# Kernel tuning notes

Hardware: AMD Instinct MI355X
Metric: run time of the kernel (lower is better)

Reference implementation:

```python
import jax, jax.numpy as jnp
import numpy as np

EPS = 1e-10


def setup_inputs() -> dict:
    key = jax.random.key(0)
    ks = jax.random.split(key, 8)
    N, C, H, W = 32, 512, 14, 14
    D, HID = 2048, 256
    s1 = 1.0 / np.sqrt(C + D)
    s2 = 1.0 / np.sqrt(HID)
    return {
        "local_feature": jax.random.normal(ks[0], (N, C, H, W), jnp.float32),
        "global_feature": jax.random.normal(ks[1], (N, D, 1, 1), jnp.float32),
        "W1": jax.random.normal(ks[2], (C + D, HID), jnp.float32) * s1,
        "b1": jnp.zeros((HID,), jnp.float32),
        "W2": jax.random.normal(ks[3], (HID, HID), jnp.float32) * s2,
        "b2": jnp.zeros((HID,), jnp.float32),
        "W3": jax.random.normal(ks[4], (HID, 1), jnp.float32) * s2,
        "b3": jnp.zeros((1,), jnp.float32),
    }


def reference(local_feature, global_feature, W1, b1, W2, b2, W3, b3):
    # Vectorized form of DMIEstimator.calculate_mi (the per-sample Python loop
    # collapsed into one batched pass with a block-diagonal negative mask).
    N, C, H, W = local_feature.shape
    hw = H * W
    nhw = N * hw
    D = global_feature.shape[1]

    lf = jnp.transpose(local_feature, (0, 2, 3, 1)).reshape(nhw, C)   # [nhw, C]
    gf = global_feature[:, :, 0, 0]                                   # [N, D]

    # combined = cat([global, local], -1); split the first Linear accordingly
    # so the [N*nhw, C+D] concat tensor is never materialized.
    h_loc = lf @ W1[D:]                        # [nhw, HID]
    h_glb = gf @ W1[:D] + b1                   # [N, HID]
    h1 = jax.nn.relu(h_glb[:, None, :] + h_loc[None, :, :])  # [N, nhw, HID]
    h2 = jax.nn.relu(h1 @ W2 + b2)                            # [N, nhw, HID]
    scores = (h2 @ W3)[..., 0] + b3[0]                        # [N, nhw]

    mx = jnp.max(scores, axis=1, keepdims=True)               # [N, 1]
    ex = jnp.exp(scores - mx)

    # negatives for sample i exclude its own hw block [hw*i, hw*(i+1))
    own = (jnp.arange(nhw)[None, :] // hw) == jnp.arange(N)[:, None]  # [N, nhw]
    neg_mean = jnp.where(own, 0.0, ex).sum(axis=1) / (nhw - hw) + EPS  # [N]

    # positive (diagonal) block of scores: scores[i, hw*i : hw*(i+1)]
    pos = scores.reshape(N, N, hw)[jnp.arange(N), jnp.arange(N)]       # [N, hw]

    mi = pos - mx - jnp.log(neg_mean)[:, None]                         # [N, hw]
    return mi.reshape(N, H, W)
```

## Files before the change

kernel.cpp:

```cpp
#include <hip/hip_runtime.h>
#include <math.h>

#define NB   32
#define CC   512
#define DD   2048
#define HWP  196
#define NHW  6272
#define HID  256

typedef _Float16 h8 __attribute__((ext_vector_type(8)));
typedef _Float16 h4 __attribute__((ext_vector_type(4)));
typedef float    f4 __attribute__((ext_vector_type(4)));
union F4H8 { f4 f; h8 h; };

__device__ __forceinline__ int fragIdx(int j, int k) {
    return ((j >> 6) << 14) + (((k >> 5) * 4 + ((j & 63) >> 4)) << 9)
         + (((((k >> 3) & 3) << 4) + (j & 15)) << 3) + (k & 7);
}

__global__ __launch_bounds__(256) void prep_kernel(const float* __restrict__ lf,
                                                   const float* __restrict__ gf,
                                                   const float* __restrict__ W1,
                                                   const float* __restrict__ W2,
                                                   float* __restrict__ hpart,
                                                   _Float16* __restrict__ W2F,
                                                   _Float16* __restrict__ W1F,
                                                   _Float16* __restrict__ lf16T) {
    int bid = blockIdx.x, tid = threadIdx.x;
    if (bid < 512) {
        int i = bid >> 4, ky = bid & 15, k = tid;
        const float* g = gf + (size_t)i * DD + ky * 128;
        const float* w = W1 + (size_t)(ky * 128) * HID + k;
        float a0 = 0.f, a1 = 0.f, a2 = 0.f, a3 = 0.f;
        #pragma unroll 8
        for (int r = 0; r < 128; r += 4) {
            a0 = fmaf(g[r + 0], w[(size_t)(r + 0) * HID], a0);
            a1 = fmaf(g[r + 1], w[(size_t)(r + 1) * HID], a1);
            a2 = fmaf(g[r + 2], w[(size_t)(r + 2) * HID], a2);
            a3 = fmaf(g[r + 3], w[(size_t)(r + 3) * HID], a3);
        }
        hpart[((size_t)i * 16 + ky) * HID + k] = (a0 + a1) + (a2 + a3);
    } else if (bid < 608) {
        int tg = (bid - 512) * 256 + tid;
        if (tg < 8192) {
            int t = tg, F = t >> 6, l = t & 63;
            int k2t = F >> 3, ks = F & 7;
            int kb = ks * 32 + (l >> 4) * 8;
            int n  = k2t * 16 + (l & 15);
            _Float16* o = W2F + (size_t)t * 8;
            #pragma unroll
            for (int j = 0; j < 8; j++) o[j] = (_Float16)W2[(size_t)(kb + j) * HID + n];
        } else {
            int t = tg - 8192, F = t >> 6, l = t & 63;
            int k2t = F >> 4, ks = F & 15;
            int kb = ks * 32 + (l >> 4) * 8;
            int n  = k2t * 16 + (l & 15);
            const float* W1c = W1 + (size_t)DD * HID;
            _Float16* o = W1F + (size_t)t * 8;
            #pragma unroll
            for (int j = 0; j < 8; j++) o[j] = (_Float16)W1c[(size_t)(kb + j) * HID + n];
        }
    } else {
        __shared__ _Float16 sT[64][HWP + 4];
        int b = bid - 608;
        int n = b >> 3, c0 = (b & 7) * 64;
        for (int task = tid; task < 64 * 49; task += 256) {
            int c = task / 49, f = task - c * 49;
            f4 v = *(const f4*)&lf[((size_t)n * CC + c0 + c) * HWP + f * 4];
            h4 o = { (_Float16)v.x, (_Float16)v.y, (_Float16)v.z, (_Float16)v.w };
            *(h4*)&sT[c][f * 4] = o;
        }
        __syncthreads();
        for (int task = tid; task < 8 * HWP; task += 256) {
            int ch = task / HWP, p = task - ch * HWP;
            h8 o;
            #pragma unroll
            for (int cc = 0; cc < 8; cc++) o[cc] = sT[ch * 8 + cc][p];
            *(h8*)&lf16T[((size_t)(n * HWP + p)) * CC + c0 + ch * 8] = o;
        }
    }
}

__global__ __launch_bounds__(256, 2) void hlocF_kernel(const _Float16* __restrict__ lf16T,
                                                       const _Float16* __restrict__ W1F,
                                                       const float* __restrict__ hpart,
                                                       const float* __restrict__ b1,
                                                       _Float16* __restrict__ g16,
                                                       _Float16* __restrict__ hF) {
    if (blockIdx.x == 196) {
        int kh = blockIdx.y;
        for (int x = threadIdx.x; x < 16 * HID; x += 256) {
            int i = kh * 16 + (x >> 8), k = x & 255;
            float s = b1[k];
            #pragma unroll
            for (int ky = 0; ky < 16; ky++) s += hpart[((size_t)i * 16 + ky) * HID + k];
            g16[(size_t)i * HID + k] = (_Float16)s;
        }
        return;
    }
    __shared__ _Float16 sLf[32][CC + 16];
    int tid = threadIdx.x;
    int w = tid >> 6, l = tid & 63, quad = l >> 4, ln = l & 15;
    int j0 = blockIdx.x * 32;
    int khalf = blockIdx.y;

    #pragma unroll
    for (int s = 0; s < 8; s++) {
        int y = s * 256 + tid;
        int row = y >> 6, col = (y & 63) * 8;
        h8 v = *(const h8*)&lf16T[(size_t)(j0 + row) * CC + col];
        *(h8*)&sLf[row][col] = v;
    }

    F4H8 Af[32];
    {
        const f4* src = (const f4*)W1F + l;
        #pragma unroll
        for (int mt = 0; mt < 2; mt++)
            #pragma unroll
            for (int ks = 0; ks < 16; ks++)
                Af[mt * 16 + ks].f = src[(size_t)((khalf * 8 + w * 2 + mt) * 16 + ks) * 64];
    }
    __syncthreads();

    f4 acc[4] = {};
    #pragma unroll
    for (int ks = 0; ks < 16; ks++) {
        h8 bF[2];
        #pragma unroll
        for (int nt = 0; nt < 2; nt++)
            bF[nt] = *(const h8*)&sLf[nt * 16 + ln][ks * 32 + quad * 8];
        #pragma unroll
        for (int mt = 0; mt < 2; mt++)
            #pragma unroll
            for (int nt = 0; nt < 2; nt++)
                acc[mt * 2 + nt] = __builtin_amdgcn_mfma_f32_16x16x32_f16(Af[mt * 16 + ks].h, bF[nt], acc[mt * 2 + nt], 0, 0, 0);
    }

    #pragma unroll
    for (int mt = 0; mt < 2; mt++)
        #pragma unroll
        for (int nt = 0; nt < 2; nt++) {
            int j  = j0 + nt * 16 + ln;
            int k2 = khalf * 128 + w * 32 + mt * 16 + quad * 4;
            h4 o = { (_Float16)acc[mt * 2 + nt][0], (_Float16)acc[mt * 2 + nt][1],
                     (_Float16)acc[mt * 2 + nt][2], (_Float16)acc[mt * 2 + nt][3] };
            *(h4*)&hF[fragIdx(j, k2)] = o;
        }
}

__global__ __launch_bounds__(1024, 2)
void score_kernel(const _Float16* __restrict__ hF,
                  const _Float16* __restrict__ g16,
                  const _Float16* __restrict__ W2F,
                  const float* __restrict__ b2,
                  const float* __restrict__ W3,
                  const float* __restrict__ b3,
                  float* __restrict__ scores) {
    __shared__ _Float16 sA[64 * HID];
    __shared__ float sRed[16][68];
    int tid = threadIdx.x, w = tid >> 6, l = tid & 63, quad = l >> 4, ln = l & 15;
    int i0 = blockIdx.x * 2, jt = blockIdx.y;

    F4H8 Af[8];
    {
        const f4* src = (const f4*)W2F + l;
        #pragma unroll
        for (int ks = 0; ks < 8; ks++)
            Af[ks].f = src[(size_t)(w * 8 + ks) * 64];
    }
    const _Float16* hbase = hF + (size_t)jt * 16384;
    float bias3 = b3[0];
    h8 z = {};

    #pragma unroll 1
    for (int ii = 0; ii < 2; ii++) {
        int i = i0 + ii;
        const _Float16* gbase = g16 + (size_t)i * HID;

        #pragma unroll
        for (int s = 0; s < 2; s++) {
            int y = s * 1024 + tid;
            h8 hv = *(const h8*)&hbase[y * 8];
            h8 gq = *(const h8*)&gbase[(y >> 8) * 32 + ((y >> 4) & 3) * 8];
            *(h8*)&sA[y * 8] = __builtin_elementwise_max(hv + gq, z);
        }
        __syncthreads();

        #pragma unroll 1
        for (int pass = 0; pass < 2; pass++) {
            f4 acc[2];
            {
                f4 bv = *(const f4*)&b2[w * 16 + quad * 4];
                acc[0] = bv;
                acc[1] = bv;
            }
            #pragma unroll
            for (int ks = 0; ks < 8; ks++) {
                #pragma unroll
                for (int nt = 0; nt < 2; nt++) {
                    int ntg = pass * 2 + nt;
                    h8 hz = *(const h8*)&sA[(ks * 4 + ntg) * 512 + l * 8];
                    acc[nt] = __builtin_amdgcn_mfma_f32_16x16x32_f16(Af[ks].h, hz, acc[nt], 0, 0, 0);
                }
            }
            {
                f4 w3v = *(const f4*)&W3[w * 16 + quad * 4];
                #pragma unroll
                for (int nt = 0; nt < 2; nt++) {
                    float s = fmaxf(acc[nt][0], 0.f) * w3v.x
                            + fmaxf(acc[nt][1], 0.f) * w3v.y
                            + fmaxf(acc[nt][2], 0.f) * w3v.z
                            + fmaxf(acc[nt][3], 0.f) * w3v.w;
                    s += __shfl_xor(s, 16, 64);
                    s += __shfl_xor(s, 32, 64);
                    if (quad == 0) sRed[w][(pass * 2 + nt) * 16 + ln] = s;
                }
            }
        }
        __syncthreads();
        if (tid < 64) {
            float s = bias3;
            #pragma unroll
            for (int ww = 0; ww < 16; ww++) s += sRed[ww][tid];
            scores[(size_t)i * NHW + jt * 64 + tid] = s;
        }
    }
}

__global__ __launch_bounds__(1024) void reduce_kernel(const float* __restrict__ scores,
                                                      float* __restrict__ out) {
    int i = blockIdx.x, tid = threadIdx.x;
    const float* row = scores + (size_t)i * NHW;
    const f4* row4 = (const f4*)row;
    __shared__ float sM[16], sT[16], sO[16], sval[1];
    int q0 = i * 49, q1 = q0 + 49;
    float m = -1e30f, t = 0.f, o = 0.f;
    for (int q = tid; q < 1568; q += 1024) {
        f4 v = row4[q];
        float vm = fmaxf(fmaxf(v.x, v.y), fmaxf(v.z, v.w));
        float nm = fmaxf(m, vm);
        float sc = expf(m - nm);
        float e = expf(v.x - nm) + expf(v.y - nm) + expf(v.z - nm) + expf(v.w - nm);
        t = t * sc + e;
        o *= sc;
        if (q >= q0 && q < q1) o += e;
        m = nm;
    }
    #pragma unroll
    for (int off = 32; off > 0; off >>= 1) {
        float m2 = __shfl_xor(m, off, 64);
        float t2 = __shfl_xor(t, off, 64);
        float o2 = __shfl_xor(o, off, 64);
        float nm = fmaxf(m, m2);
        float sa = expf(m - nm), sb = expf(m2 - nm);
        t = t * sa + t2 * sb;
        o = o * sa + o2 * sb;
        m = nm;
    }
    if ((tid & 63) == 0) { sM[tid >> 6] = m; sT[tid >> 6] = t; sO[tid >> 6] = o; }
    __syncthreads();
    if (tid == 0) {
        float M = sM[0], T = sT[0], O = sO[0];
        for (int c = 1; c < 16; c++) {
            float nm = fmaxf(M, sM[c]);
            float sa = expf(M - nm), sb = expf(sM[c] - nm);
            T = T * sa + sT[c] * sb;
            O = O * sa + sO[c] * sb;
            M = nm;
        }
        float neg_mean = (T - O) / (float)(NHW - HWP) + 1e-10f;
        sval[0] = M + logf(neg_mean);
    }
    __syncthreads();
    float sub = sval[0];
    if (tid < HWP) out[(size_t)i * HWP + tid] = row[i * HWP + tid] - sub;
}

extern "C" void kernel_launch(void* const* d_in, const int* in_sizes, int n_in,
                              void* d_out, int out_size, void* d_ws, size_t ws_size,
                              hipStream_t stream) {
    const float* lf = (const float*)d_in[0];
    const float* gf = (const float*)d_in[1];
    const float* W1 = (const float*)d_in[2];
    const float* b1 = (const float*)d_in[3];
    const float* W2 = (const float*)d_in[4];
    const float* b2 = (const float*)d_in[5];
    const float* W3 = (const float*)d_in[6];
    const float* b3 = (const float*)d_in[7];
    float* out = (float*)d_out;

    char* ws = (char*)d_ws;
    _Float16* hF     = (_Float16*)ws;
    _Float16* g16    = (_Float16*)(ws + 3211264);
    _Float16* W2F    = (_Float16*)(ws + 3227648);
    _Float16* W1F    = (_Float16*)(ws + 3358720);
    _Float16* lf16T  = (_Float16*)(ws + 3620864);
    float*    scores = (float*)   (ws + 10043392);
    float*    hpart  = (float*)   (ws + 10846208);

    hipLaunchKernelGGL(prep_kernel, dim3(864), dim3(256), 0, stream,
                       lf, gf, W1, W2, hpart, W2F, W1F, lf16T);
    hipLaunchKernelGGL(hlocF_kernel, dim3(197, 2), dim3(256), 0, stream,
                       lf16T, W1F, hpart, b1, g16, hF);
    hipLaunchKernelGGL(score_kernel, dim3(16, 98), dim3(1024), 0, stream,
                       hF, g16, W2F, b2, W3, b3, scores);
    hipLaunchKernelGGL(reduce_kernel, dim3(NB), dim3(1024), 0, stream, scores, out);
}
```

Measured before the change: 137.9 us.

## Switch score kernel to 32x32x16 MFMA with 4 waves and row-major hidden layout

The score kernel now uses 256-thread blocks, where each wave holds 64 output channels of W2 in registers as 32x32x16 MFMA fragments. Before, it used 1024 threads with 16x16x32 MFMAs at 16 channels per wave. The local hidden activations are stored row-major, and the h1 tile is reshuffled into the MFMA B-fragment layout in shared memory. Bias b2 is added in the epilogue, and the cross-wave reduction shrinks from 16 partials to 4. The aim is more MFMA work per LDS read and less reduction and sync overhead, at the cost of heavier register pressure (32 A fragments per thread) and fewer threads per block.

```diff
diff --git a/kernel.cpp b/kernel.cpp
--- a/kernel.cpp
+++ b/kernel.cpp
@@ -11,19 +11,15 @@
 typedef _Float16 h8 __attribute__((ext_vector_type(8)));
 typedef _Float16 h4 __attribute__((ext_vector_type(4)));
 typedef float    f4 __attribute__((ext_vector_type(4)));
+typedef float    f16v __attribute__((ext_vector_type(16)));
 union F4H8 { f4 f; h8 h; };
-
-__device__ __forceinline__ int fragIdx(int j, int k) {
-    return ((j >> 6) << 14) + (((k >> 5) * 4 + ((j & 63) >> 4)) << 9)
-         + (((((k >> 3) & 3) << 4) + (j & 15)) << 3) + (k & 7);
-}
 
 __global__ __launch_bounds__(256) void prep_kernel(const float* __restrict__ lf,
                                                    const float* __restrict__ gf,
                                                    const float* __restrict__ W1,
                                                    const float* __restrict__ W2,
                                                    float* __restrict__ hpart,
-                                                   _Float16* __restrict__ W2F,
+                                                   _Float16* __restrict__ W2G,
                                                    _Float16* __restrict__ W1F,
                                                    _Float16* __restrict__ lf16T) {
     int bid = blockIdx.x, tid = threadIdx.x;
@@ -44,10 +40,10 @@
         int tg = (bid - 512) * 256 + tid;
         if (tg < 8192) {
             int t = tg, F = t >> 6, l = t & 63;
-            int k2t = F >> 3, ks = F & 7;
-            int kb = ks * 32 + (l >> 4) * 8;
-            int n  = k2t * 16 + (l & 15);
-            _Float16* o = W2F + (size_t)t * 8;
+            int mt2 = F >> 4, ks = F & 15;
+            int kb = ks * 16 + (l >> 5) * 8;
+            int n  = mt2 * 32 + (l & 31);
+            _Float16* o = W2G + (size_t)t * 8;
             #pragma unroll
             for (int j = 0; j < 8; j++) o[j] = (_Float16)W2[(size_t)(kb + j) * HID + n];
         } else {
@@ -86,7 +82,7 @@
                                                        const float* __restrict__ hpart,
                                                        const float* __restrict__ b1,
                                                        _Float16* __restrict__ g16,
-                                                       _Float16* __restrict__ hF) {
+                                                       _Float16* __restrict__ hL) {
     if (blockIdx.x == 196) {
         int kh = blockIdx.y;
         for (int x = threadIdx.x; x < 16 * HID; x += 256) {
@@ -145,85 +141,85 @@
             int k2 = khalf * 128 + w * 32 + mt * 16 + quad * 4;
             h4 o = { (_Float16)acc[mt * 2 + nt][0], (_Float16)acc[mt * 2 + nt][1],
                      (_Float16)acc[mt * 2 + nt][2], (_Float16)acc[mt * 2 + nt][3] };
-            *(h4*)&hF[fragIdx(j, k2)] = o;
-        }
-}
-
-__global__ __launch_bounds__(1024, 2)
-void score_kernel(const _Float16* __restrict__ hF,
+            *(h4*)&hL[(size_t)j * HID + k2] = o;
+        }
+}
+
+__global__ __launch_bounds__(256, 2)
+void score_kernel(const _Float16* __restrict__ hL,
                   const _Float16* __restrict__ g16,
-                  const _Float16* __restrict__ W2F,
+                  const _Float16* __restrict__ W2G,
                   const float* __restrict__ b2,
                   const float* __restrict__ W3,
                   const float* __restrict__ b3,
                   float* __restrict__ scores) {
-    __shared__ _Float16 sA[64 * HID];
-    __shared__ float sRed[16][68];
-    int tid = threadIdx.x, w = tid >> 6, l = tid & 63, quad = l >> 4, ln = l & 15;
+    __shared__ _Float16 sB[64 * HID];
+    __shared__ float sRed[4][68];
+    int tid = threadIdx.x, w = tid >> 6, l = tid & 63;
+    int hi = l >> 5, ln32 = l & 31;
     int i0 = blockIdx.x * 2, jt = blockIdx.y;
-
-    F4H8 Af[8];
+    int j0 = jt * 64;
+
+    F4H8 Af[2][16];
     {
-        const f4* src = (const f4*)W2F + l;
-        #pragma unroll
-        for (int ks = 0; ks < 8; ks++)
-            Af[ks].f = src[(size_t)(w * 8 + ks) * 64];
-    }
-    const _Float16* hbase = hF + (size_t)jt * 16384;
+        const f4* src = (const f4*)W2G + l;
+        #pragma unroll
+        for (int a = 0; a < 2; a++)
+            #pragma unroll
+            for (int ks = 0; ks < 16; ks++)
+                Af[a][ks].f = src[(size_t)((w * 2 + a) * 16 + ks) * 64];
+    }
     float bias3 = b3[0];
-    h8 z = {};
+
+    int sj = tid >> 2, so = (tid & 3) * 8;
+    const _Float16* hrow = hL + ((size_t)(j0 + sj)) * HID + so * 8;
 
     #pragma unroll 1
     for (int ii = 0; ii < 2; ii++) {
         int i = i0 + ii;
-        const _Float16* gbase = g16 + (size_t)i * HID;
-
-        #pragma unroll
-        for (int s = 0; s < 2; s++) {
-            int y = s * 1024 + tid;
-            h8 hv = *(const h8*)&hbase[y * 8];
-            h8 gq = *(const h8*)&gbase[(y >> 8) * 32 + ((y >> 4) & 3) * 8];
-            *(h8*)&sA[y * 8] = __builtin_elementwise_max(hv + gq, z);
+        const _Float16* grow = g16 + (size_t)i * HID + so * 8;
+        h8 z = {};
+        #pragma unroll
+        for (int oi = 0; oi < 8; oi++) {
+            int o = so + oi;
+            h8 hv = *(const h8*)&hrow[oi * 8];
+            h8 gq = *(const h8*)&grow[oi * 8];
+            h8 h1 = __builtin_elementwise_max(hv + gq, z);
+            int cell = ((sj >> 5) * 16 + (o >> 1)) * 512 + ((o & 1) * 32 + (sj & 31)) * 8;
+            *(h8*)&sB[cell] = h1;
         }
         __syncthreads();
 
         #pragma unroll 1
-        for (int pass = 0; pass < 2; pass++) {
-            f4 acc[2];
-            {
-                f4 bv = *(const f4*)&b2[w * 16 + quad * 4];
-                acc[0] = bv;
-                acc[1] = bv;
+        for (int ntg = 0; ntg < 2; ntg++) {
+            f16v acc[2] = {};
+            #pragma unroll
+            for (int ks = 0; ks < 16; ks++) {
+                h8 bz = *(const h8*)&sB[((ntg * 16 + ks) * 64 + l) * 8];
+                acc[0] = __builtin_amdgcn_mfma_f32_32x32x16_f16(Af[0][ks].h, bz, acc[0], 0, 0, 0);
+                acc[1] = __builtin_amdgcn_mfma_f32_32x32x16_f16(Af[1][ks].h, bz, acc[1], 0, 0, 0);
             }
-            #pragma unroll
-            for (int ks = 0; ks < 8; ks++) {
+            float s = 0.f;
+            #pragma unroll
+            for (int a = 0; a < 2; a++) {
+                int kb = w * 64 + a * 32 + 4 * hi;
                 #pragma unroll
-                for (int nt = 0; nt < 2; nt++) {
-                    int ntg = pass * 2 + nt;
-                    h8 hz = *(const h8*)&sA[(ks * 4 + ntg) * 512 + l * 8];
-                    acc[nt] = __builtin_amdgcn_mfma_f32_16x16x32_f16(Af[ks].h, hz, acc[nt], 0, 0, 0);
+                for (int q = 0; q < 4; q++) {
+                    f4 b2v = *(const f4*)&b2[kb + q * 8];
+                    f4 w3v = *(const f4*)&W3[kb + q * 8];
+                    s += fmaxf(acc[a][q * 4 + 0] + b2v.x, 0.f) * w3v.x
+                       + fmaxf(acc[a][q * 4 + 1] + b2v.y, 0.f) * w3v.y
+                       + fmaxf(acc[a][q * 4 + 2] + b2v.z, 0.f) * w3v.z
+                       + fmaxf(acc[a][q * 4 + 3] + b2v.w, 0.f) * w3v.w;
                 }
             }
-            {
-                f4 w3v = *(const f4*)&W3[w * 16 + quad * 4];
-                #pragma unroll
-                for (int nt = 0; nt < 2; nt++) {
-                    float s = fmaxf(acc[nt][0], 0.f) * w3v.x
-                            + fmaxf(acc[nt][1], 0.f) * w3v.y
-                            + fmaxf(acc[nt][2], 0.f) * w3v.z
-                            + fmaxf(acc[nt][3], 0.f) * w3v.w;
-                    s += __shfl_xor(s, 16, 64);
-                    s += __shfl_xor(s, 32, 64);
-                    if (quad == 0) sRed[w][(pass * 2 + nt) * 16 + ln] = s;
-                }
-            }
+            s += __shfl_xor(s, 32, 64);
+            if (hi == 0) sRed[w][ntg * 32 + ln32] = s;
         }
         __syncthreads();
         if (tid < 64) {
-            float s = bias3;
-            #pragma unroll
-            for (int ww = 0; ww < 16; ww++) s += sRed[ww][tid];
-            scores[(size_t)i * NHW + jt * 64 + tid] = s;
+            scores[(size_t)i * NHW + j0 + tid] =
+                sRed[0][tid] + sRed[1][tid] + sRed[2][tid] + sRed[3][tid] + bias3;
         }
     }
 }
@@ -291,19 +287,19 @@
     float* out = (float*)d_out;
 
     char* ws = (char*)d_ws;
-    _Float16* hF     = (_Float16*)ws;
+    _Float16* hL     = (_Float16*)ws;
     _Float16* g16    = (_Float16*)(ws + 3211264);
-    _Float16* W2F    = (_Float16*)(ws + 3227648);
+    _Float16* W2G    = (_Float16*)(ws + 3227648);
     _Float16* W1F    = (_Float16*)(ws + 3358720);
     _Float16* lf16T  = (_Float16*)(ws + 3620864);
     float*    scores = (float*)   (ws + 10043392);
     float*    hpart  = (float*)   (ws + 10846208);
 
     hipLaunchKernelGGL(prep_kernel, dim3(864), dim3(256), 0, stream,
-                       lf, gf, W1, W2, hpart, W2F, W1F, lf16T);
+                       lf, gf, W1, W2, hpart, W2G, W1F, lf16T);
     hipLaunchKernelGGL(hlocF_kernel, dim3(197, 2), dim3(256), 0, stream,
-                       lf16T, W1F, hpart, b1, g16, hF);
-    hipLaunchKernelGGL(score_kernel, dim3(16, 98), dim3(1024), 0, stream,
-                       hF, g16, W2F, b2, W3, b3, scores);
+                       lf16T, W1F, hpart, b1, g16, hL);
+    hipLaunchKernelGGL(score_kernel, dim3(16, 98), dim3(256), 0, stream,
+                       hL, g16, W2G, b2, W3, b3, scores);
     hipLaunchKernelGGL(reduce_kernel, dim3(NB), dim3(1024), 0, stream, scores, out);
 }
```

After: 148.0 us. 1.07x slower.
